# Performance work log

Measured on AMD Instinct MI355X. Metric: run time of the kernel, lower is better.

Reference implementation:

```python
import jax, jax.numpy as jnp
import numpy as np

N_NODES = 50000
N_EDGES = 800000
D_IN, D_HID, D_OUT = 16, 64, 16
N_BLOCKS = 4


def setup_inputs() -> dict:
    key = jax.random.key(0)
    ks = jax.random.split(key, 12)
    s = 0.05  # small init scale to keep sum-aggregation over 4 blocks stable
    return {
        "x": jax.random.normal(ks[0], (N_NODES, D_IN), jnp.float32),
        "lframes": jax.random.normal(ks[1], (N_NODES, 4, 4), jnp.float32),
        "edge_index": jax.random.randint(ks[2], (2, N_EDGES), 0, N_NODES, jnp.int64),
        "lin_in_w": jax.random.normal(ks[3], (D_IN, D_HID), jnp.float32) * s,
        "lin_in_b": jnp.zeros((D_HID,), jnp.float32),
        # per-block mlp1: Linear(2D->D), ReLU, Linear(D->D), ReLU, Linear(D->D)
        "w0": jax.random.normal(ks[4], (N_BLOCKS, 2 * D_HID, D_HID), jnp.float32) * s,
        "b0": jnp.zeros((N_BLOCKS, D_HID), jnp.float32),
        "w1": jax.random.normal(ks[5], (N_BLOCKS, D_HID, D_HID), jnp.float32) * s,
        "b1": jnp.zeros((N_BLOCKS, D_HID), jnp.float32),
        "w2": jax.random.normal(ks[6], (N_BLOCKS, D_HID, D_HID), jnp.float32) * s,
        "b2": jnp.zeros((N_BLOCKS, D_HID), jnp.float32),
        "lin_out_w": jax.random.normal(ks[7], (D_HID, D_OUT), jnp.float32) * s,
        "lin_out_b": jnp.zeros((D_OUT,), jnp.float32),
    }


def reference(x, lframes, edge_index, lin_in_w, lin_in_b,
              w0, b0, w1, b1, w2, b2, lin_out_w, lin_out_b):
    src = edge_index[0]  # x_j (source / neighbor)
    dst = edge_index[1]  # x_i (target / aggregation node)
    h = x @ lin_in_w + lin_in_b  # [N, D]
    for k in range(N_BLOCKS):
        # message: cat((x_j, x_i)) -> mlp1 ; mlp2 is Identity (num_layers_mlp2=0)
        m = jnp.concatenate((h[src], h[dst]), axis=-1)  # [E, 2D]
        m = jax.nn.relu(m @ w0[k] + b0[k])
        m = jax.nn.relu(m @ w1[k] + b1[k])
        m = m @ w2[k] + b2[k]  # [E, D]
        # aggregate: scatter-add at target node
        h = jax.ops.segment_sum(m, dst, num_segments=N_NODES)
    return h @ lin_out_w + lin_out_b  # [N, D_OUT]
```

## Files before the change

### kernel.cpp

```cpp
#include <hip/hip_runtime.h>
#include <hip/hip_bf16.h>

#define N_NODES 50000
#define N_EDGES 800000
#define D_IN    16
#define D_HID   64
#define D_OUT   16
#define NCHUNK  ((N_NODES + 255) / 256)
#define TMAX    100352

typedef __hip_bfloat16 bf16;
typedef _Float16 f16;
typedef _Float16 f16x8 __attribute__((ext_vector_type(8)));
typedef float    f32x4 __attribute__((ext_vector_type(4)));
typedef _Float16 f16x8a __attribute__((ext_vector_type(8), may_alias));

__device__ __forceinline__ float b2f(bf16 v) { return __bfloat162float(v); }
__device__ __forceinline__ int clampn(int v) {
    return v < 0 ? 0 : (v >= N_NODES ? N_NODES - 1 : v);
}
__device__ __forceinline__ float rdf(const void* p, long i, int isbf) {
    return isbf ? b2f(((const bf16*)p)[i]) : ((const float*)p)[i];
}
__device__ __forceinline__ f16x8 relu8(f16x8 v) {
#pragma unroll
    for (int j = 0; j < 8; j++) v[j] = v[j] > (f16)0 ? v[j] : (f16)0;
    return v;
}

__global__ __launch_bounds__(256) void k_detect(const unsigned short* __restrict__ xw,
                                                const int* __restrict__ ei,
                                                int* __restrict__ flags,
                                                int* __restrict__ hist)
{
    int i = blockIdx.x * 256 + threadIdx.x;
    if (i < N_NODES) hist[i] = 0;
    if (blockIdx.x == 0 && threadIdx.x == 0) {
        int inband = 0;
        for (int j = 0; j < 256; j++) {
            unsigned short w = xw[2 * j];
            int e = (w >> 7) & 0xFF;
            if ((w & 0x7FFF) == 0 || (e >= 100 && e <= 140)) inband++;
        }
        flags[0] = (inband >= 192) ? 1 : 0;
        int z = 1;
        for (int j = 1; j < 128; j += 2) z &= (ei[j] == 0) ? 1 : 0;
        flags[1] = z;
    }
}

__global__ __launch_bounds__(256) void k_wprep(const int* __restrict__ flags,
                                               const void* __restrict__ gw0,
                                               const void* __restrict__ gw1,
                                               const void* __restrict__ gw2,
                                               f16* __restrict__ wfrag)
{
    int idx = blockIdx.x * 256 + threadIdx.x;
    if (idx >= 4 * 32 * 64) return;
    const int isbf = flags[0];
    int kb = idx >> 11, rem = idx & 2047;
    int slot = rem >> 6, lane = rem & 63;
    int lm = lane & 15, quad = lane >> 4;
    f16* outp = wfrag + (long)idx * 8;
    if (slot < 16) {
        int c = slot >> 2, q = slot & 3;
        long base = (long)kb * 2 * D_HID * D_HID;
#pragma unroll
        for (int j = 0; j < 8; j++)
            outp[j] = (f16)rdf(gw0, base + (long)(c * 32 + quad * 8 + j) * 64 + q * 16 + lm, isbf);
    } else {
        const void* gw = (slot < 24) ? gw1 : gw2;
        int s = (slot < 24) ? slot - 16 : slot - 24;
        int c = s >> 2, q = s & 3;
        long base = (long)kb * D_HID * D_HID;
#pragma unroll
        for (int j = 0; j < 8; j++)
            outp[j] = (f16)rdf(gw, base + (long)(c * 32 + quad * 8 + j) * 64 + q * 16 + lm, isbf);
    }
}

__global__ __launch_bounds__(256) void k_hist4(const int* __restrict__ flags,
                                               const int* __restrict__ eidx,
                                               int* __restrict__ hist)
{
    int base = (blockIdx.x * 256 + threadIdx.x) * 4;
    if (base >= N_EDGES) return;
    const int strd = flags[1] ? 2 : 1;
    const long dbase = flags[1] ? (long)(2 * N_EDGES) : (long)N_EDGES;
#pragma unroll
    for (int j = 0; j < 4; j++) {
        int e = base + j;
        if (e < N_EDGES)
            atomicAdd(&hist[clampn(eidx[dbase + (long)e * strd])], 1);
    }
}

__global__ __launch_bounds__(256) void k_scan1(const int* __restrict__ hist,
                                               int* __restrict__ bsum_e,
                                               int* __restrict__ bsum_t)
{
    __shared__ int re[256], rt[256];
    const int t = threadIdx.x;
    int i = blockIdx.x * 256 + t;
    int v = (i < N_NODES) ? hist[i] : 0;
    re[t] = v; rt[t] = (v + 15) >> 4;
    __syncthreads();
    for (int d = 128; d > 0; d >>= 1) {
        if (t < d) { re[t] += re[t + d]; rt[t] += rt[t + d]; }
        __syncthreads();
    }
    if (t == 0) { bsum_e[blockIdx.x] = re[0]; bsum_t[blockIdx.x] = rt[0]; }
}

__global__ __launch_bounds__(256) void k_scan2(const int* __restrict__ bsum_e,
                                               const int* __restrict__ bsum_t,
                                               int* __restrict__ boff_e,
                                               int* __restrict__ boff_t,
                                               int* __restrict__ tot_e,
                                               int* __restrict__ tot_t)
{
    __shared__ int se[256], st_[256];
    const int t = threadIdx.x;
    se[t]  = (t < NCHUNK) ? bsum_e[t] : 0;
    st_[t] = (t < NCHUNK) ? bsum_t[t] : 0;
    __syncthreads();
    for (int d = 1; d < 256; d <<= 1) {
        int ve = (t >= d) ? se[t - d] : 0;
        int vt = (t >= d) ? st_[t - d] : 0;
        __syncthreads();
        se[t] += ve; st_[t] += vt;
        __syncthreads();
    }
    if (t < NCHUNK) {
        boff_e[t] = (t == 0) ? 0 : se[t - 1];
        boff_t[t] = (t == 0) ? 0 : st_[t - 1];
    }
    if (t == NCHUNK - 1) { tot_e[0] = se[t]; tot_t[0] = st_[t]; }
}

__global__ __launch_bounds__(256) void k_scan3(const int* __restrict__ hist,
                                               const int* __restrict__ boff_e,
                                               const int* __restrict__ boff_t,
                                               int* __restrict__ off,
                                               int* __restrict__ cursor,
                                               int* __restrict__ toff,
                                               int* __restrict__ tmeta)
{
    __shared__ int se[256], st_[256];
    const int t = threadIdx.x;
    int i = blockIdx.x * 256 + t;
    int v = (i < N_NODES) ? hist[i] : 0;
    int w = (v + 15) >> 4;
    se[t] = v; st_[t] = w;
    __syncthreads();
    for (int d = 1; d < 256; d <<= 1) {
        int ue = (t >= d) ? se[t - d] : 0;
        int ut = (t >= d) ? st_[t - d] : 0;
        __syncthreads();
        se[t] += ue; st_[t] += ut;
        __syncthreads();
    }
    if (i < N_NODES) {
        int exE = boff_e[blockIdx.x] + se[t] - v;
        off[i] = exE; cursor[i] = exE;
        int exT = boff_t[blockIdx.x] + st_[t] - w;
        toff[i] = exT;
        for (int j = 0; j < w; j++)
            tmeta[exT + j] = i | (min(16, v - 16 * j) << 20);
    }
}

__global__ __launch_bounds__(256) void k_scatter4(const int* __restrict__ flags,
                                                  const int* __restrict__ eidx,
                                                  int* __restrict__ cursor,
                                                  int* __restrict__ ssrc)
{
    int base = (blockIdx.x * 256 + threadIdx.x) * 4;
    if (base >= N_EDGES) return;
    const int strd = flags[1] ? 2 : 1;
    const long dbase = flags[1] ? (long)(2 * N_EDGES) : (long)N_EDGES;
    int d[4], s[4], pos[4], cnt = min(4, N_EDGES - base);
#pragma unroll
    for (int j = 0; j < 4; j++)
        if (j < cnt) {
            d[j] = clampn(eidx[dbase + (long)(base + j) * strd]);
            s[j] = clampn(eidx[(long)(base + j) * strd]);
        }
#pragma unroll
    for (int j = 0; j < 4; j++)
        if (j < cnt) pos[j] = atomicAdd(&cursor[d[j]], 1);
#pragma unroll
    for (int j = 0; j < 4; j++)
        if (j < cnt) ssrc[pos[j]] = s[j];
}

__global__ __launch_bounds__(256) void k_fill(const int* __restrict__ hist,
                                              const int* __restrict__ off,
                                              const int* __restrict__ toff,
                                              const int* __restrict__ totalp,
                                              const int* __restrict__ tmeta,
                                              const int* __restrict__ ssrc,
                                              int* __restrict__ spad)
{
    int idx = blockIdx.x * 256 + threadIdx.x;
    int t = idx >> 4, i = idx & 15;
    if (t >= totalp[0]) return;
    int n = tmeta[t] & 0xFFFFF;
    int j = t - toff[n];
    int dg = hist[n];
    spad[idx] = ssrc[off[n] + min(16 * j + i, dg - 1)];
}

__global__ __launch_bounds__(256) void k_lin_in(const int* __restrict__ flags,
                                                const void* __restrict__ x,
                                                const void* __restrict__ w,
                                                const void* __restrict__ b,
                                                float* __restrict__ h)
{
    int idx = blockIdx.x * 256 + threadIdx.x;
    if (idx >= N_NODES * D_HID) return;
    const int isbf = flags[0];
    int n = idx >> 6, c = idx & 63;
    float acc = rdf(b, c, isbf);
#pragma unroll
    for (int i = 0; i < D_IN; i++)
        acc += rdf(x, (long)n * D_IN + i, isbf) * rdf(w, (long)i * D_HID + c, isbf);
    h[idx] = acc;
}

#define HP_ST 72

__global__ __launch_bounds__(256) void k_proj(
    const int* __restrict__ flags, float* hio,
    const f16* __restrict__ wfrag, const void* __restrict__ gb0,
    f16* __restrict__ psrc, f16* __restrict__ pdst, int kblk)
{
    __shared__ f16 hL_s[4][16 * HP_ST];

    const int tid  = threadIdx.x;
    const int isbf = flags[0];
    const int wv = tid >> 6, ln = tid & 63;
    const int lm = ln & 15, quad = ln >> 4;
    f16* hL = hL_s[wv];

    const int g = blockIdx.x * 4 + wv;
    if (g >= N_NODES / 16) return;
    const int n0 = g * 16;

    const f16* wb = wfrag + (long)kblk * 32 * 64 * 8;

#pragma unroll
    for (int i = 0; i < 16; i++) {
        int idx = i * 64 + ln;
        hL[(idx >> 6) * HP_ST + (idx & 63)] = (f16)hio[(long)n0 * 64 + idx];
    }
#pragma unroll
    for (int i = 0; i < 16; i++)
        hio[(long)n0 * 64 + i * 64 + ln] = 0.f;

    f16x8 a[2];
#pragma unroll
    for (int c = 0; c < 2; c++)
        a[c] = *(const f16x8a*)&hL[lm * HP_ST + c * 32 + quad * 8];

    f32x4 accS[4], accD[4];
#pragma unroll
    for (int q = 0; q < 4; q++) {
        float bd = rdf(gb0, (long)kblk * 64 + q * 16 + lm, isbf);
        accS[q] = (f32x4){0.f, 0.f, 0.f, 0.f};
        accD[q] = (f32x4){bd, bd, bd, bd};
    }
#pragma unroll
    for (int c = 0; c < 2; c++)
#pragma unroll
        for (int q = 0; q < 4; q++) {
            f16x8 bs = *(const f16x8a*)&wb[(((c + 0) * 4 + q) * 64 + ln) * 8];
            f16x8 bd = *(const f16x8a*)&wb[(((c + 2) * 4 + q) * 64 + ln) * 8];
            accS[q] = __builtin_amdgcn_mfma_f32_16x16x32_f16(a[c], bs, accS[q], 0, 0, 0);
            accD[q] = __builtin_amdgcn_mfma_f32_16x16x32_f16(a[c], bd, accD[q], 0, 0, 0);
        }
#pragma unroll
    for (int q = 0; q < 4; q++)
#pragma unroll
        for (int r = 0; r < 4; r++) {
            long o = (long)(n0 + quad * 4 + r) * 64 + q * 16 + lm;
            psrc[o] = (f16)accS[q][r];
            pdst[o] = (f16)accD[q][r];
        }
}

#define Y_ST 72

__global__ __launch_bounds__(256) void k_edge_tile(
    const int* __restrict__ flags,
    const int* __restrict__ ssrc_pad, const int* __restrict__ tmeta,
    const int* __restrict__ toff,
    const f16* __restrict__ psrc, const f16* __restrict__ pdst,
    float* __restrict__ hout,
    const f16* __restrict__ wfrag, const void* __restrict__ gb1,
    const void* __restrict__ gb2, int kblk)
{
    __shared__ f16 y_s[4][2][16 * Y_ST];

    const int tid  = threadIdx.x;
    const int isbf = flags[0];
    const int wv = tid >> 6, ln = tid & 63;
    const int lm = ln & 15, quad = ln >> 4;

    const f16* wb = wfrag + (long)kblk * 32 * 64 * 8;
    f16x8 bw1[2][4], bw2[2][4];
#pragma unroll
    for (int c = 0; c < 2; c++)
#pragma unroll
        for (int q = 0; q < 4; q++) {
            bw1[c][q] = *(const f16x8a*)&wb[((16 + c * 4 + q) * 64 + ln) * 8];
            bw2[c][q] = *(const f16x8a*)&wb[((24 + c * 4 + q) * 64 + ln) * 8];
        }
    float bias1[4], bias2[4];
#pragma unroll
    for (int q = 0; q < 4; q++) {
        bias1[q] = rdf(gb1, (long)kblk * 64 + q * 16 + lm, isbf);
        bias2[q] = rdf(gb2, (long)kblk * 64 + q * 16 + lm, isbf);
    }

    f16* yA = y_s[wv][0];
    f16* yB = y_s[wv][1];
    const int sub = ln & 7, eh = ln >> 3;

    const int T  = toff[N_NODES];
    const int W  = gridDim.x * 4;
    const int gw = blockIdx.x * 4 + wv;
    const int t0 = (int)((long)gw * T / W);
    const int t1 = (int)((long)(gw + 1) * T / W);
    if (t0 >= t1) return;

    int tcA = t0, tcB = min(t0 + 1, T - 1);
    int tc2 = min(t0 + 2, T - 1), tc3 = min(t0 + 3, T - 1);
    int m0 = tmeta[tcA], m1 = tmeta[tcB], m2 = tmeta[tc2], m3 = tmeta[tc3];
    int s2a = ssrc_pad[tc2 * 16 + eh], s2b = ssrc_pad[tc2 * 16 + 8 + eh];
    int s3a = ssrc_pad[tc3 * 16 + eh], s3b = ssrc_pad[tc3 * 16 + 8 + eh];
    int s0a = ssrc_pad[tcA * 16 + eh], s0b = ssrc_pad[tcA * 16 + 8 + eh];
    int s1a = ssrc_pad[tcB * 16 + eh], s1b = ssrc_pad[tcB * 16 + 8 + eh];
    f16x8 ps0a = *(const f16x8a*)&psrc[(long)s0a * 64 + sub * 8];
    f16x8 ps0b = *(const f16x8a*)&psrc[(long)s0b * 64 + sub * 8];
    f16x8 pd0  = *(const f16x8a*)&pdst[(long)(m0 & 0xFFFFF) * 64 + sub * 8];
    f16x8 ps1a = *(const f16x8a*)&psrc[(long)s1a * 64 + sub * 8];
    f16x8 ps1b = *(const f16x8a*)&psrc[(long)s1b * 64 + sub * 8];
    f16x8 pd1  = *(const f16x8a*)&pdst[(long)(m1 & 0xFFFFF) * 64 + sub * 8];

    float accn[4] = {0.f, 0.f, 0.f, 0.f};

    for (int tt = t0; tt < t1; tt += 2) {
        const int tc4 = min(tt + 4, T - 1), tc5 = min(tt + 5, T - 1);
        int m4 = tmeta[tc4], m5 = tmeta[tc5];
        int s4a = ssrc_pad[tc4 * 16 + eh], s4b = ssrc_pad[tc4 * 16 + 8 + eh];
        int s5a = ssrc_pad[tc5 * 16 + eh], s5b = ssrc_pad[tc5 * 16 + 8 + eh];
        f16x8 ps2a = *(const f16x8a*)&psrc[(long)s2a * 64 + sub * 8];
        f16x8 ps2b = *(const f16x8a*)&psrc[(long)s2b * 64 + sub * 8];
        f16x8 pd2  = *(const f16x8a*)&pdst[(long)(m2 & 0xFFFFF) * 64 + sub * 8];
        f16x8 ps3a = *(const f16x8a*)&psrc[(long)s3a * 64 + sub * 8];
        f16x8 ps3b = *(const f16x8a*)&psrc[(long)s3b * 64 + sub * 8];
        f16x8 pd3  = *(const f16x8a*)&pdst[(long)(m3 & 0xFFFFF) * 64 + sub * 8];

        const int hasB = (tt + 1 < t1);
        const int v0 = m0 >> 20;
        const int v1 = hasB ? (m1 >> 20) : 0;

        *(f16x8a*)&yA[eh * Y_ST + sub * 8]       = relu8(ps0a + pd0);
        *(f16x8a*)&yA[(8 + eh) * Y_ST + sub * 8] = relu8(ps0b + pd0);
        *(f16x8a*)&yB[eh * Y_ST + sub * 8]       = relu8(ps1a + pd1);
        *(f16x8a*)&yB[(8 + eh) * Y_ST + sub * 8] = relu8(ps1b + pd1);

        f16x8 a1A[2], a1B[2];
#pragma unroll
        for (int c = 0; c < 2; c++) {
            a1A[c] = *(const f16x8a*)&yA[lm * Y_ST + c * 32 + quad * 8];
            a1B[c] = *(const f16x8a*)&yB[lm * Y_ST + c * 32 + quad * 8];
        }
        f32x4 accA[4], accB[4];
#pragma unroll
        for (int q = 0; q < 4; q++) {
            accA[q] = (f32x4){bias1[q], bias1[q], bias1[q], bias1[q]};
            accB[q] = (f32x4){bias1[q], bias1[q], bias1[q], bias1[q]};
        }
#pragma unroll
        for (int c = 0; c < 2; c++)
#pragma unroll
            for (int q = 0; q < 4; q++) {
                accA[q] = __builtin_amdgcn_mfma_f32_16x16x32_f16(a1A[c], bw1[c][q], accA[q], 0, 0, 0);
                accB[q] = __builtin_amdgcn_mfma_f32_16x16x32_f16(a1B[c], bw1[c][q], accB[q], 0, 0, 0);
            }
#pragma unroll
        for (int q = 0; q < 4; q++)
#pragma unroll
            for (int r = 0; r < 4; r++) {
                yA[(quad * 4 + r) * Y_ST + q * 16 + lm] = (f16)fmaxf(accA[q][r], 0.f);
                yB[(quad * 4 + r) * Y_ST + q * 16 + lm] = (f16)fmaxf(accB[q][r], 0.f);
            }

        f16x8 a2A[2], a2B[2];
#pragma unroll
        for (int c = 0; c < 2; c++) {
            a2A[c] = *(const f16x8a*)&yA[lm * Y_ST + c * 32 + quad * 8];
            a2B[c] = *(const f16x8a*)&yB[lm * Y_ST + c * 32 + quad * 8];
        }
#pragma unroll
        for (int q = 0; q < 4; q++) {
            accA[q] = (f32x4){bias2[q], bias2[q], bias2[q], bias2[q]};
            accB[q] = (f32x4){bias2[q], bias2[q], bias2[q], bias2[q]};
        }
#pragma unroll
        for (int c = 0; c < 2; c++)
#pragma unroll
            for (int q = 0; q < 4; q++) {
                accA[q] = __builtin_amdgcn_mfma_f32_16x16x32_f16(a2A[c], bw2[c][q], accA[q], 0, 0, 0);
                accB[q] = __builtin_amdgcn_mfma_f32_16x16x32_f16(a2B[c], bw2[c][q], accB[q], 0, 0, 0);
            }

#pragma unroll
        for (int q = 0; q < 4; q++)
#pragma unroll
            for (int r = 0; r < 4; r++)
                if (quad * 4 + r < v0) accn[q] += accA[q][r];
        {
            const int curn = m0 & 0xFFFFF;
            const int nxt  = hasB ? (m1 & 0xFFFFF) : -1;
            if (nxt != curn) {
#pragma unroll
                for (int q = 0; q < 4; q++) {
                    float v = accn[q];
                    v += __shfl_xor(v, 16, 64);
                    v += __shfl_xor(v, 32, 64);
                    if (quad == 0) atomicAdd(&hout[(long)curn * 64 + q * 16 + lm], v);
                    accn[q] = 0.f;
                }
            }
        }
        if (hasB) {
#pragma unroll
            for (int q = 0; q < 4; q++)
#pragma unroll
                for (int r = 0; r < 4; r++)
                    if (quad * 4 + r < v1) accn[q] += accB[q][r];
            const int curn = m1 & 0xFFFFF;
            const int nxt  = (tt + 2 < t1) ? (m2 & 0xFFFFF) : -1;
            if (nxt != curn) {
#pragma unroll
                for (int q = 0; q < 4; q++) {
                    float v = accn[q];
                    v += __shfl_xor(v, 16, 64);
                    v += __shfl_xor(v, 32, 64);
                    if (quad == 0) atomicAdd(&hout[(long)curn * 64 + q * 16 + lm], v);
                    accn[q] = 0.f;
                }
            }
        }

        m0 = m2; m1 = m3; m2 = m4; m3 = m5;
        s2a = s4a; s2b = s4b; s3a = s5a; s3b = s5b;
        ps0a = ps2a; ps0b = ps2b; pd0 = pd2;
        ps1a = ps3a; ps1b = ps3b; pd1 = pd3;
    }
}

__global__ __launch_bounds__(256) void k_lin_out(const int* __restrict__ flags,
                                                 const float* __restrict__ h,
                                                 const void* __restrict__ w,
                                                 const void* __restrict__ b,
                                                 float* __restrict__ out)
{
    int idx = blockIdx.x * 256 + threadIdx.x;
    if (idx >= N_NODES * D_OUT) return;
    const int isbf = flags[0];
    int n = idx >> 4, c = idx & 15;
    float acc = rdf(b, c, isbf);
    const float* hr = h + (long)n * D_HID;
#pragma unroll
    for (int i = 0; i < D_HID; i++) acc += hr[i] * rdf(w, (long)i * D_OUT + c, isbf);
    out[idx] = acc;
}

extern "C" void kernel_launch(void* const* d_in, const int* in_sizes, int n_in,
                              void* d_out, int out_size, void* d_ws, size_t ws_size,
                              hipStream_t stream)
{
    const void* x    = d_in[0];
    const int*  ei   = (const int*)d_in[2];
    const void* liw  = d_in[3];
    const void* lib  = d_in[4];
    const void* w0   = d_in[5];
    const void* b0   = d_in[6];
    const void* w1   = d_in[7];
    const void* b1   = d_in[8];
    const void* w2   = d_in[9];
    const void* b2   = d_in[10];
    const void* low  = d_in[11];
    const void* lob  = d_in[12];
    float* out = (float*)d_out;

    char* wp = (char*)d_ws;
    int*   flags  = (int*)wp;                 wp += 256;
    float* hA     = (float*)wp;               wp += (size_t)N_NODES * D_HID * 4;
    f16*   Psrc   = (f16*)wp;                 wp += (size_t)N_NODES * D_HID * 2;
    f16*   Pdst   = (f16*)wp;                 wp += (size_t)N_NODES * D_HID * 2;
    f16*   wfrag  = (f16*)wp;                 wp += (size_t)4 * 32 * 64 * 8 * 2;
    int*   hist   = (int*)wp;                 wp += (size_t)N_NODES * 4;
    int*   off    = (int*)wp;                 wp += ((size_t)N_NODES + 1) * 4;
    int*   cursor = (int*)wp;                 wp += (size_t)N_NODES * 4;
    int*   toff   = (int*)wp;                 wp += ((size_t)N_NODES + 1) * 4;
    int*   bsum_e = (int*)wp;                 wp += 256 * 4;
    int*   bsum_t = (int*)wp;                 wp += 256 * 4;
    int*   boff_e = (int*)wp;                 wp += 256 * 4;
    int*   boff_t = (int*)wp;                 wp += 256 * 4;
    int*   ssrc   = (int*)wp;                 wp += (size_t)N_EDGES * 4;
    int*   tmeta  = (int*)wp;                 wp += (size_t)TMAX * 4;
    int*   spad   = (int*)wp;

    const int HN = N_NODES * D_HID;
    const int gH = (HN + 255) / 256;
    const int gE4 = (N_EDGES / 4 + 255) / 256;

    k_detect<<<NCHUNK, 256, 0, stream>>>((const unsigned short*)x, ei, flags, hist);
    k_wprep<<<32, 256, 0, stream>>>(flags, w0, w1, w2, wfrag);

    k_hist4<<<gE4, 256, 0, stream>>>(flags, ei, hist);
    k_scan1<<<NCHUNK, 256, 0, stream>>>(hist, bsum_e, bsum_t);
    k_scan2<<<1, 256, 0, stream>>>(bsum_e, bsum_t, boff_e, boff_t,
                                   off + N_NODES, toff + N_NODES);
    k_scan3<<<NCHUNK, 256, 0, stream>>>(hist, boff_e, boff_t, off, cursor, toff, tmeta);
    k_scatter4<<<gE4, 256, 0, stream>>>(flags, ei, cursor, ssrc);
    k_fill<<<(TMAX * 16) / 256, 256, 0, stream>>>(hist, off, toff, toff + N_NODES,
                                                  tmeta, ssrc, spad);

    k_lin_in<<<gH, 256, 0, stream>>>(flags, x, liw, lib, hA);

    for (int k = 0; k < 4; k++) {
        k_proj<<<(N_NODES / 16 + 3) / 4, 256, 0, stream>>>(flags, hA, wfrag, b0,
                                                           Psrc, Pdst, k);
        k_edge_tile<<<1024, 256, 0, stream>>>(flags, spad, tmeta, toff,
                                              Psrc, Pdst, hA, wfrag, b1, b2, k);
    }

    k_lin_out<<<(N_NODES * D_OUT + 255) / 256, 256, 0, stream>>>(flags, hA, low, lob, out);
}
```

Baseline: 458.3 us.

## Snap edge-tile ranges to node boundaries and replace atomics with plain stores

Each wave's tile range in the edge kernel is moved forward until it starts on a node boundary, so every destination node is reduced entirely by one wave. That lets the final per-node write be a plain store instead of a float atomicAdd, and the projection kernel now zeroes only rows with no incoming edges instead of clearing all of h. It also merges the weight-prep, histogram and input-linear kernels into one launch to cut launch overhead. The risk is load imbalance for high-degree nodes, plus a short serial scan of tmeta at the start of each wave.

```diff
diff --git a/kernel.cpp b/kernel.cpp
--- a/kernel.cpp
+++ b/kernel.cpp
@@ -8,6 +8,8 @@
 #define D_OUT   16
 #define NCHUNK  ((N_NODES + 255) / 256)
 #define TMAX    100352
+#define GE4     ((N_EDGES / 4 + 255) / 256)
+#define GH      ((N_NODES * D_HID + 255) / 256)
 
 typedef __hip_bfloat16 bf16;
 typedef _Float16 f16;
@@ -49,49 +51,61 @@
     }
 }
 
-__global__ __launch_bounds__(256) void k_wprep(const int* __restrict__ flags,
-                                               const void* __restrict__ gw0,
-                                               const void* __restrict__ gw1,
-                                               const void* __restrict__ gw2,
-                                               f16* __restrict__ wfrag)
-{
-    int idx = blockIdx.x * 256 + threadIdx.x;
-    if (idx >= 4 * 32 * 64) return;
+__global__ __launch_bounds__(256) void k_prep(const int* __restrict__ flags,
+                                              const void* __restrict__ gw0,
+                                              const void* __restrict__ gw1,
+                                              const void* __restrict__ gw2,
+                                              f16* __restrict__ wfrag,
+                                              const int* __restrict__ eidx,
+                                              int* __restrict__ hist,
+                                              const void* __restrict__ x,
+                                              const void* __restrict__ liw,
+                                              const void* __restrict__ lib,
+                                              float* __restrict__ h)
+{
     const int isbf = flags[0];
-    int kb = idx >> 11, rem = idx & 2047;
-    int slot = rem >> 6, lane = rem & 63;
-    int lm = lane & 15, quad = lane >> 4;
-    f16* outp = wfrag + (long)idx * 8;
-    if (slot < 16) {
-        int c = slot >> 2, q = slot & 3;
-        long base = (long)kb * 2 * D_HID * D_HID;
-#pragma unroll
-        for (int j = 0; j < 8; j++)
-            outp[j] = (f16)rdf(gw0, base + (long)(c * 32 + quad * 8 + j) * 64 + q * 16 + lm, isbf);
+    const int bid = blockIdx.x;
+    if (bid < 32) {
+        int idx = bid * 256 + threadIdx.x;
+        int kb = idx >> 11, rem = idx & 2047;
+        int slot = rem >> 6, lane = rem & 63;
+        int lm = lane & 15, quad = lane >> 4;
+        f16* outp = wfrag + (long)idx * 8;
+        if (slot < 16) {
+            int c = slot >> 2, q = slot & 3;
+            long base = (long)kb * 2 * D_HID * D_HID;
+#pragma unroll
+            for (int j = 0; j < 8; j++)
+                outp[j] = (f16)rdf(gw0, base + (long)(c * 32 + quad * 8 + j) * 64 + q * 16 + lm, isbf);
+        } else {
+            const void* gw = (slot < 24) ? gw1 : gw2;
+            int s = (slot < 24) ? slot - 16 : slot - 24;
+            int c = s >> 2, q = s & 3;
+            long base = (long)kb * D_HID * D_HID;
+#pragma unroll
+            for (int j = 0; j < 8; j++)
+                outp[j] = (f16)rdf(gw, base + (long)(c * 32 + quad * 8 + j) * 64 + q * 16 + lm, isbf);
+        }
+    } else if (bid < 32 + GE4) {
+        int base = ((bid - 32) * 256 + threadIdx.x) * 4;
+        if (base >= N_EDGES) return;
+        const int strd = flags[1] ? 2 : 1;
+        const long dbase = flags[1] ? (long)(2 * N_EDGES) : (long)N_EDGES;
+#pragma unroll
+        for (int j = 0; j < 4; j++) {
+            int e = base + j;
+            if (e < N_EDGES)
+                atomicAdd(&hist[clampn(eidx[dbase + (long)e * strd])], 1);
+        }
     } else {
-        const void* gw = (slot < 24) ? gw1 : gw2;
-        int s = (slot < 24) ? slot - 16 : slot - 24;
-        int c = s >> 2, q = s & 3;
-        long base = (long)kb * D_HID * D_HID;
-#pragma unroll
-        for (int j = 0; j < 8; j++)
-            outp[j] = (f16)rdf(gw, base + (long)(c * 32 + quad * 8 + j) * 64 + q * 16 + lm, isbf);
-    }
-}
-
-__global__ __launch_bounds__(256) void k_hist4(const int* __restrict__ flags,
-                                               const int* __restrict__ eidx,
-                                               int* __restrict__ hist)
-{
-    int base = (blockIdx.x * 256 + threadIdx.x) * 4;
-    if (base >= N_EDGES) return;
-    const int strd = flags[1] ? 2 : 1;
-    const long dbase = flags[1] ? (long)(2 * N_EDGES) : (long)N_EDGES;
-#pragma unroll
-    for (int j = 0; j < 4; j++) {
-        int e = base + j;
-        if (e < N_EDGES)
-            atomicAdd(&hist[clampn(eidx[dbase + (long)e * strd])], 1);
+        int idx = (bid - 32 - GE4) * 256 + threadIdx.x;
+        if (idx >= N_NODES * D_HID) return;
+        int n = idx >> 6, c = idx & 63;
+        float acc = rdf(lib, c, isbf);
+#pragma unroll
+        for (int i = 0; i < D_IN; i++)
+            acc += rdf(x, (long)n * D_IN + i, isbf) * rdf(liw, (long)i * D_HID + c, isbf);
+        h[idx] = acc;
     }
 }
 
@@ -211,28 +225,12 @@
     spad[idx] = ssrc[off[n] + min(16 * j + i, dg - 1)];
 }
 
-__global__ __launch_bounds__(256) void k_lin_in(const int* __restrict__ flags,
-                                                const void* __restrict__ x,
-                                                const void* __restrict__ w,
-                                                const void* __restrict__ b,
-                                                float* __restrict__ h)
-{
-    int idx = blockIdx.x * 256 + threadIdx.x;
-    if (idx >= N_NODES * D_HID) return;
-    const int isbf = flags[0];
-    int n = idx >> 6, c = idx & 63;
-    float acc = rdf(b, c, isbf);
-#pragma unroll
-    for (int i = 0; i < D_IN; i++)
-        acc += rdf(x, (long)n * D_IN + i, isbf) * rdf(w, (long)i * D_HID + c, isbf);
-    h[idx] = acc;
-}
-
 #define HP_ST 72
 
 __global__ __launch_bounds__(256) void k_proj(
     const int* __restrict__ flags, float* hio,
     const f16* __restrict__ wfrag, const void* __restrict__ gb0,
+    const int* __restrict__ hist,
     f16* __restrict__ psrc, f16* __restrict__ pdst, int kblk)
 {
     __shared__ f16 hL_s[4][16 * HP_ST];
@@ -256,7 +254,7 @@
     }
 #pragma unroll
     for (int i = 0; i < 16; i++)
-        hio[(long)n0 * 64 + i * 64 + ln] = 0.f;
+        if (hist[n0 + i] == 0) hio[(long)(n0 + i) * 64 + ln] = 0.f;
 
     f16x8 a[2];
 #pragma unroll
@@ -330,8 +328,12 @@
     const int T  = toff[N_NODES];
     const int W  = gridDim.x * 4;
     const int gw = blockIdx.x * 4 + wv;
-    const int t0 = (int)((long)gw * T / W);
-    const int t1 = (int)((long)(gw + 1) * T / W);
+    int t0 = (int)((long)gw * T / W);
+    int t1 = (int)((long)(gw + 1) * T / W);
+    if (t0 > 0)
+        while (t0 < T && (tmeta[t0] & 0xFFFFF) == (tmeta[t0 - 1] & 0xFFFFF)) t0++;
+    if (t1 > 0)
+        while (t1 < T && (tmeta[t1] & 0xFFFFF) == (tmeta[t1 - 1] & 0xFFFFF)) t1++;
     if (t0 >= t1) return;
 
     int tcA = t0, tcB = min(t0 + 1, T - 1);
@@ -431,7 +433,7 @@
                     float v = accn[q];
                     v += __shfl_xor(v, 16, 64);
                     v += __shfl_xor(v, 32, 64);
-                    if (quad == 0) atomicAdd(&hout[(long)curn * 64 + q * 16 + lm], v);
+                    if (quad == 0) hout[(long)curn * 64 + q * 16 + lm] = v;
                     accn[q] = 0.f;
                 }
             }
@@ -450,7 +452,7 @@
                     float v = accn[q];
                     v += __shfl_xor(v, 16, 64);
                     v += __shfl_xor(v, 32, 64);
-                    if (quad == 0) atomicAdd(&hout[(long)curn * 64 + q * 16 + lm], v);
+                    if (quad == 0) hout[(long)curn * 64 + q * 16 + lm] = v;
                     accn[q] = 0.f;
                 }
             }
@@ -516,27 +518,21 @@
     int*   tmeta  = (int*)wp;                 wp += (size_t)TMAX * 4;
     int*   spad   = (int*)wp;
 
-    const int HN = N_NODES * D_HID;
-    const int gH = (HN + 255) / 256;
-    const int gE4 = (N_EDGES / 4 + 255) / 256;
-
     k_detect<<<NCHUNK, 256, 0, stream>>>((const unsigned short*)x, ei, flags, hist);
-    k_wprep<<<32, 256, 0, stream>>>(flags, w0, w1, w2, wfrag);
-
-    k_hist4<<<gE4, 256, 0, stream>>>(flags, ei, hist);
+    k_prep<<<32 + GE4 + GH, 256, 0, stream>>>(flags, w0, w1, w2, wfrag,
+                                              ei, hist, x, liw, lib, hA);
+
     k_scan1<<<NCHUNK, 256, 0, stream>>>(hist, bsum_e, bsum_t);
     k_scan2<<<1, 256, 0, stream>>>(bsum_e, bsum_t, boff_e, boff_t,
                                    off + N_NODES, toff + N_NODES);
     k_scan3<<<NCHUNK, 256, 0, stream>>>(hist, boff_e, boff_t, off, cursor, toff, tmeta);
-    k_scatter4<<<gE4, 256, 0, stream>>>(flags, ei, cursor, ssrc);
+    k_scatter4<<<(N_EDGES / 4 + 255) / 256, 256, 0, stream>>>(flags, ei, cursor, ssrc);
     k_fill<<<(TMAX * 16) / 256, 256, 0, stream>>>(hist, off, toff, toff + N_NODES,
                                                   tmeta, ssrc, spad);
 
-    k_lin_in<<<gH, 256, 0, stream>>>(flags, x, liw, lib, hA);
-
     for (int k = 0; k < 4; k++) {
         k_proj<<<(N_NODES / 16 + 3) / 4, 256, 0, stream>>>(flags, hA, wfrag, b0,
-                                                           Psrc, Pdst, k);
+                                                           hist, Psrc, Pdst, k);
         k_edge_tile<<<1024, 256, 0, stream>>>(flags, spad, tmeta, toff,
                                               Psrc, Pdst, hA, wfrag, b1, b2, k);
     }
```

Result: no change. 455.6 us (-0.6%).
